# Performance work log

Hardware: AMD Instinct MI355X
Metric: run time of the kernel (lower is better)

## Reference

```python
import jax, jax.numpy as jnp
import numpy as np

EMBED_DIM = 1024
NUM_HEADS = 16
HEAD_DIM = EMBED_DIM // NUM_HEADS
BATCH, SEQ = 1, 4096


def setup_inputs() -> dict:
    key = jax.random.key(0)
    k1, k2, k3 = jax.random.split(key, 3)
    hidden_states = jax.random.normal(k1, (BATCH, SEQ, EMBED_DIM), dtype=jnp.float32)
    W_qkv = jax.random.normal(k2, (3 * EMBED_DIM, EMBED_DIM), dtype=jnp.float32) * 0.02
    b_qkv = jnp.zeros((3 * EMBED_DIM,), dtype=jnp.float32)
    # torch init: identity per head, perturb slightly to make test non-trivial
    eye = jnp.broadcast_to(jnp.eye(HEAD_DIM, dtype=jnp.float32), (NUM_HEADS, HEAD_DIM, HEAD_DIM))
    hebbian_trace = eye + 0.01 * jax.random.normal(k3, (NUM_HEADS, HEAD_DIM, HEAD_DIM), dtype=jnp.float32)
    return {"hidden_states": hidden_states, "W_qkv": W_qkv, "b_qkv": b_qkv, "hebbian_trace": hebbian_trace}


def reference(hidden_states, W_qkv, b_qkv, hebbian_trace):
    B, S, E = hidden_states.shape
    H, D = NUM_HEADS, HEAD_DIM
    qkv = hidden_states @ W_qkv.T + b_qkv              # [B,S,3E]
    q, k, v = jnp.split(qkv, 3, axis=-1)
    # [B,H,S,D]
    q = q.reshape(B, S, H, D).transpose(0, 2, 1, 3)
    k = k.reshape(B, S, H, D).transpose(0, 2, 1, 3)
    v = v.reshape(B, S, H, D).transpose(0, 2, 1, 3)
    scores = jnp.einsum('bhqd,bhkd->bhqk', q, k) / jnp.sqrt(jnp.float32(D))
    attn = jax.nn.softmax(scores, axis=-1)
    weighted_v = jnp.einsum('bhqk,bhkd->bhqd', attn, v)  # [B,H,S,D]
    # torch einsum 'blhd,hdd->blhd': repeated 'd' in trace -> diagonal scaling
    wv = weighted_v.transpose(0, 2, 1, 3)               # [B,S,H,D]
    v_transformed = jnp.einsum('blhd,hdd->blhd', wv, hebbian_trace)
    return v_transformed.reshape(B, S, E)
```

## Files before the change

kernel.cpp:

```cpp
#include <hip/hip_runtime.h>
#include <hip/hip_bf16.h>
#include <stdint.h>

#define S_LEN 4096

typedef short s16x8  __attribute__((ext_vector_type(8)));
typedef float f32x4  __attribute__((ext_vector_type(4)));
typedef float f32x16 __attribute__((ext_vector_type(16)));

#define CEXP 0.18033688011112042f

__device__ __forceinline__ unsigned short f2bf(float f) {
    union { float f; unsigned u; } v; v.f = f;
    unsigned r = v.u + 0x7fffu + ((v.u >> 16) & 1u);
    return (unsigned short)(r >> 16);
}

__device__ __forceinline__ ushort2 pkbf(float a, float b) {
    float2 f; f.x = a; f.y = b;
    __hip_bfloat162 h = __float22bfloat162_rn(f);
    union { __hip_bfloat162 h; ushort2 u; } cv; cv.h = h;
    return cv.u;
}

__device__ __forceinline__ ushort4 pkbf4(float x, float y, float z, float w) {
    ushort2 lo = pkbf(x, y), hi = pkbf(z, w);
    ushort4 r; r.x = lo.x; r.y = lo.y; r.z = hi.x; r.w = hi.y;
    return r;
}

__device__ __forceinline__ unsigned pku(float a, float b) {
    union { ushort2 s; unsigned u; } c; c.s = pkbf(a, b); return c.u;
}

typedef const __attribute__((address_space(1))) void* gas_t;
typedef __attribute__((address_space(3))) void* sas_t;

__device__ __forceinline__ void async16(const void* g, void* s) {
    __builtin_amdgcn_global_load_lds((gas_t)g, (sas_t)s, 16, 0, 0);
}

__global__ __launch_bounds__(256) void cvt_bf16(
    const float* __restrict__ X, const float* __restrict__ W,
    unsigned short* __restrict__ Xb, unsigned short* __restrict__ Wb)
{
    const long NX = 4194304;
    long i = (long)(blockIdx.x * 256 + threadIdx.x) * 8;
    const float* src; unsigned short* dst; long off;
    if (i < NX) { src = X; dst = Xb; off = i; }
    else        { src = W; dst = Wb; off = i - NX; }
    float4 a = *(const float4*)(src + off);
    float4 b = *(const float4*)(src + off + 4);
    union { s16x8 v; ushort4 q[2]; } o;
    o.q[0] = pkbf4(a.x, a.y, a.z, a.w);
    o.q[1] = pkbf4(b.x, b.y, b.z, b.w);
    *(s16x8*)(dst + off) = o.v;
}

__global__ __launch_bounds__(256) void qkv_gemm_bf16(
    const unsigned short* __restrict__ Xb, const unsigned short* __restrict__ Wb,
    const float* __restrict__ bias, const float* __restrict__ trace,
    unsigned short* __restrict__ Qb, unsigned short* __restrict__ Kb,
    unsigned short* __restrict__ Vt)
{
    __shared__ __align__(16) unsigned short sm[17408];
    unsigned short* As = sm;
    unsigned short* Bs = sm + 8192;

    const int t = threadIdx.x;
    const int l = t & 63;
    const int w = t >> 6;
    const int bm = blockIdx.y, bn = blockIdx.x;
    const int rowBase = (w >> 1) * 64;
    const int colBase = (w & 1) * 64;

    f32x4 acc[4][4];
#pragma unroll
    for (int i = 0; i < 4; i++)
#pragma unroll
        for (int j = 0; j < 4; j++) acc[i][j] = (f32x4)0.f;

    const int srow = l >> 3;
    const int scol = (l & 7) * 8;

    for (int kt = 0; kt < 16; ++kt) {
        const int k0 = kt * 64;
#pragma unroll
        for (int c = 0; c < 4; ++c) {
            int m = w * 4 + c;
            const unsigned short* ga = Xb + (bm * 128 + m * 8 + srow) * 1024 + k0 + scol;
            const unsigned short* gb = Wb + (bn * 128 + m * 8 + srow) * 1024 + k0 + scol;
            async16(ga, As + m * 512);
            async16(gb, Bs + m * 512);
        }
        __syncthreads();

#pragma unroll
        for (int kc = 0; kc < 2; ++kc) {
            s16x8 af[4], bf[4];
#pragma unroll
            for (int i = 0; i < 4; i++) {
                af[i] = *(const s16x8*)(As + (rowBase + i * 16 + (l & 15)) * 64 + kc * 32 + (l >> 4) * 8);
                bf[i] = *(const s16x8*)(Bs + (colBase + i * 16 + (l & 15)) * 64 + kc * 32 + (l >> 4) * 8);
            }
#pragma unroll
            for (int i = 0; i < 4; i++)
#pragma unroll
                for (int j = 0; j < 4; j++)
                    acc[i][j] = __builtin_amdgcn_mfma_f32_16x16x32_bf16(af[i], bf[j], acc[i][j], 0, 0, 0);
        }
        __syncthreads();
    }

    if (bn < 16) {
        unsigned short* Ls = sm;
        const int region = bn >> 3;
        unsigned short* dst = region ? Kb : Qb;
        const float scl = region ? 1.0f : CEXP;
#pragma unroll
        for (int j = 0; j < 4; j++) {
            int cl = colBase + j * 16 + (l & 15);
            float bv = bias[bn * 128 + cl];
#pragma unroll
            for (int i = 0; i < 4; i++) {
                int s0 = rowBase + i * 16 + ((l >> 4) << 2);
#pragma unroll
                for (int r = 0; r < 4; r++)
                    Ls[(s0 + r) * 136 + cl] = f2bf((acc[i][j][r] + bv) * scl);
            }
        }
        __syncthreads();
#pragma unroll
        for (int p = 0; p < 8; ++p) {
            int tk = p * 256 + t;
            int s  = tk >> 4;
            int ch = tk & 15;
            int gc = bn * 128 + ch * 8;
            int h  = (gc >> 6) & 15, d = gc & 63;
            s16x8 v = *(const s16x8*)(Ls + s * 136 + ch * 8);
            *(s16x8*)(dst + (h * S_LEN + bm * 128 + s) * 64 + d) = v;
        }
    } else {
        __syncthreads();
        unsigned short* Lt = sm;
#pragma unroll
        for (int j = 0; j < 4; j++) {
            int cl = colBase + j * 16 + (l & 15);
            int o  = bn * 128 + cl - 2048;
            float bv = bias[bn * 128 + cl];
            float tr = trace[(o >> 6) * 4096 + (o & 63) * 65];
#pragma unroll
            for (int i = 0; i < 4; i++) {
                int s0 = rowBase + i * 16 + ((l >> 4) << 2);
                *(ushort4*)(Lt + cl * 136 + s0) =
                    pkbf4((acc[i][j][0] + bv) * tr, (acc[i][j][1] + bv) * tr,
                          (acc[i][j][2] + bv) * tr, (acc[i][j][3] + bv) * tr);
            }
        }
        __syncthreads();
#pragma unroll
        for (int p = 0; p < 8; ++p) {
            int dl  = (t >> 4) + p * 16;
            int sch = (t & 15) * 8;
            int o = bn * 128 + dl - 2048;
            int h = o >> 6, d = o & 63;
            s16x8 v = *(const s16x8*)(Lt + dl * 136 + sch);
            *(s16x8*)(Vt + (h * 64 + d) * S_LEN + bm * 128 + sch) = v;
        }
    }
}

__global__ __launch_bounds__(256) void qkv_gemm_f32(
    const float* __restrict__ X, const float* __restrict__ W,
    const float* __restrict__ bias, const float* __restrict__ trace,
    unsigned short* __restrict__ Qb, unsigned short* __restrict__ Kb,
    unsigned short* __restrict__ Vt)
{
    __shared__ __align__(16) unsigned short sm[17408];
    unsigned short* As = sm;
    unsigned short* Bs = sm + 5120;

    const int t = threadIdx.x;
    const int l = t & 63;
    const int w = t >> 6;
    const int bm = blockIdx.y, bn = blockIdx.x;
    const int rowBase = (w >> 1) * 64;
    const int colBase = (w & 1) * 64;

    f32x4 acc[4][4];
#pragma unroll
    for (int i = 0; i < 4; i++)
#pragma unroll
        for (int j = 0; j < 4; j++) acc[i][j] = (f32x4)0.f;

    const int sr = t >> 3;
    const int sc = (t & 7) * 4;

    for (int kt = 0; kt < 32; ++kt) {
        const int k0 = kt * 32;
#pragma unroll
        for (int p = 0; p < 4; ++p) {
            int r = sr + p * 32;
            float4 xa = *(const float4*)(X + (bm * 128 + r) * 1024 + k0 + sc);
            float4 wb = *(const float4*)(W + (bn * 128 + r) * 1024 + k0 + sc);
            *(ushort4*)(As + r * 40 + sc) = pkbf4(xa.x, xa.y, xa.z, xa.w);
            *(ushort4*)(Bs + r * 40 + sc) = pkbf4(wb.x, wb.y, wb.z, wb.w);
        }
        __syncthreads();

        s16x8 af[4], bf[4];
#pragma unroll
        for (int i = 0; i < 4; i++) {
            af[i] = *(const s16x8*)(As + (rowBase + i * 16 + (l & 15)) * 40 + (l >> 4) * 8);
            bf[i] = *(const s16x8*)(Bs + (colBase + i * 16 + (l & 15)) * 40 + (l >> 4) * 8);
        }
#pragma unroll
        for (int i = 0; i < 4; i++)
#pragma unroll
            for (int j = 0; j < 4; j++)
                acc[i][j] = __builtin_amdgcn_mfma_f32_16x16x32_bf16(af[i], bf[j], acc[i][j], 0, 0, 0);
        __syncthreads();
    }

    if (bn < 16) {
#pragma unroll
        for (int j = 0; j < 4; j++) {
            int col = bn * 128 + colBase + j * 16 + (l & 15);
            float bv = bias[col];
            int region = col >> 10;
            int within = col & 1023;
            int h = within >> 6, d = within & 63;
            unsigned short* dst = (region == 0) ? Qb : Kb;
            float scl = (region == 0) ? CEXP : 1.0f;
#pragma unroll
            for (int i = 0; i < 4; i++) {
                int s0 = bm * 128 + rowBase + i * 16 + ((l >> 4) << 2);
#pragma unroll
                for (int r = 0; r < 4; r++)
                    dst[(h * S_LEN + s0 + r) * 64 + d] = f2bf((acc[i][j][r] + bv) * scl);
            }
        }
    } else {
        __syncthreads();
        unsigned short* Lt = sm;
#pragma unroll
        for (int j = 0; j < 4; j++) {
            int cl = colBase + j * 16 + (l & 15);
            int o  = bn * 128 + cl - 2048;
            float bv = bias[bn * 128 + cl];
            float tr = trace[(o >> 6) * 4096 + (o & 63) * 65];
#pragma unroll
            for (int i = 0; i < 4; i++) {
                int s0 = rowBase + i * 16 + ((l >> 4) << 2);
                *(ushort4*)(Lt + cl * 136 + s0) =
                    pkbf4((acc[i][j][0] + bv) * tr, (acc[i][j][1] + bv) * tr,
                          (acc[i][j][2] + bv) * tr, (acc[i][j][3] + bv) * tr);
            }
        }
        __syncthreads();
#pragma unroll
        for (int p = 0; p < 8; ++p) {
            int dl  = (t >> 4) + p * 16;
            int sch = (t & 15) * 8;
            int o = bn * 128 + dl - 2048;
            int h = o >> 6, d = o & 63;
            s16x8 v = *(const s16x8*)(Lt + dl * 136 + sch);
            *(s16x8*)(Vt + (h * 64 + d) * S_LEN + bm * 128 + sch) = v;
        }
    }
}

__global__ __launch_bounds__(512, 4) void attn(
    const unsigned short* __restrict__ Qb, const unsigned short* __restrict__ Kb,
    const unsigned short* __restrict__ Vt, float* __restrict__ out)
{
    __shared__ __align__(16) unsigned short sm[34816];
    __shared__ float lArr[256];

    const int t = threadIdx.x;
    const int l = t & 63;
    const int w = t >> 6;
    const int g = w >> 2;
    const int wg = w & 3;
    const int wq = w & 3;
    const int bid = blockIdx.x;
    const int xcd = bid & 7;
    const int j   = bid >> 3;
    const int h   = xcd * 2 + (j & 1);
    const int qblk = j >> 1;
    const int qbase = qblk * 128 + wq * 32;
    const int l31 = l & 31;
    const int lh  = l >> 5;
    const int swz = l31 & 7;

    s16x8 qf[4];
#pragma unroll
    for (int ks = 0; ks < 4; ks++)
        qf[ks] = *(const s16x8*)(Qb + (h * S_LEN + qbase + l31) * 64 + ks * 16 + lh * 8);

    f32x16 O0 = (f32x16)0.f, O1 = (f32x16)0.f;
    float2 lpA; lpA.x = 0.f; lpA.y = 0.f;
    float2 lpB; lpB.x = 0.f; lpB.y = 0.f;

    const int p0 = (wg * 2 + 0) * 64 + l;
    const int p1 = (wg * 2 + 1) * 64 + l;
    const int r0_ = p0 >> 3, c0_ = (p0 & 7) ^ (r0_ & 7);
    const int r1_ = p1 >> 3, c1_ = (p1 & 7) ^ (r1_ & 7);
    const unsigned short* gk0 = Kb + (h * S_LEN + g * 2048 + r0_) * 64 + c0_ * 8;
    const unsigned short* gk1 = Kb + (h * S_LEN + g * 2048 + r1_) * 64 + c1_ * 8;
    const unsigned short* gv0 = Vt + (h * 64 + r0_) * S_LEN + g * 2048 + c0_ * 8;
    const unsigned short* gv1 = Vt + (h * 64 + r1_) * S_LEN + g * 2048 + c1_ * 8;

    {
        unsigned short* kb_ = sm + g * 8192 + wg * 1024;
        async16(gk0, kb_);
        async16(gk1, kb_ + 512);
        async16(gv0, kb_ + 4096);
        async16(gv1, kb_ + 4096 + 512);
    }

    for (int kt = 0; kt < 32; ++kt) {
        __syncthreads();
        const unsigned short* sb  = sm + ((kt & 1) * 2 + g) * 8192;
        const unsigned short* vbs = sb + 4096;

        if (kt < 31) {
            gk0 += 4096; gk1 += 4096; gv0 += 64; gv1 += 64;
            unsigned short* kb_ = sm + (((kt + 1) & 1) * 2 + g) * 8192 + wg * 1024;
            async16(gk0, kb_);
            async16(gk1, kb_ + 512);
            async16(gv0, kb_ + 4096);
            async16(gv1, kb_ + 4096 + 512);
        }

        f32x16 S0 = (f32x16)0.f, S1 = (f32x16)0.f;
        __builtin_amdgcn_s_setprio(1);
#pragma unroll
        for (int ks = 0; ks < 4; ks++) {
            const int off = ((ks * 2 + lh) ^ swz) * 8;
            s16x8 a0 = *(const s16x8*)(sb + l31 * 64 + off);
            s16x8 a1 = *(const s16x8*)(sb + (32 + l31) * 64 + off);
            S0 = __builtin_amdgcn_mfma_f32_32x32x16_bf16(a0, qf[ks], S0, 0, 0, 0);
            S1 = __builtin_amdgcn_mfma_f32_32x32x16_bf16(a1, qf[ks], S1, 0, 0, 0);
        }
        __builtin_amdgcn_s_setprio(0);

#pragma unroll
        for (int i = 0; i < 16; i += 4) {
            float p0v = __builtin_amdgcn_exp2f(S0[i+0]); S0[i+0] = p0v; lpA.x += p0v;
            float p1v = __builtin_amdgcn_exp2f(S0[i+1]); S0[i+1] = p1v; lpA.y += p1v;
            float p2v = __builtin_amdgcn_exp2f(S0[i+2]); S0[i+2] = p2v; lpB.x += p2v;
            float p3v = __builtin_amdgcn_exp2f(S0[i+3]); S0[i+3] = p3v; lpB.y += p3v;
        }
#pragma unroll
        for (int i = 0; i < 16; i += 4) {
            float p0v = __builtin_amdgcn_exp2f(S1[i+0]); S1[i+0] = p0v; lpA.x += p0v;
            float p1v = __builtin_amdgcn_exp2f(S1[i+1]); S1[i+1] = p1v; lpA.y += p1v;
            float p2v = __builtin_amdgcn_exp2f(S1[i+2]); S1[i+2] = p2v; lpB.x += p2v;
            float p3v = __builtin_amdgcn_exp2f(S1[i+3]); S1[i+3] = p3v; lpB.y += p3v;
        }

        __builtin_amdgcn_s_setprio(1);
#define PVBLK(SX, BO, KS) do {                                               \
        unsigned pa0 = pku(SX[(BO)+0], SX[(BO)+1]);                          \
        unsigned pc0 = pku(SX[(BO)+4], SX[(BO)+5]);                          \
        unsigned pa1 = pku(SX[(BO)+2], SX[(BO)+3]);                          \
        unsigned pc1 = pku(SX[(BO)+6], SX[(BO)+7]);                          \
        auto r0 = __builtin_amdgcn_permlane32_swap(pa0, pc0, false, false);  \
        auto r1 = __builtin_amdgcn_permlane32_swap(pa1, pc1, false, false);  \
        union { s16x8 v; unsigned u[4]; } pb_;                               \
        pb_.u[0] = r0[0]; pb_.u[1] = r1[0]; pb_.u[2] = r0[1]; pb_.u[3] = r1[1]; \
        const int offv = (((KS) * 2 + lh) ^ swz) * 8;                        \
        s16x8 av0 = *(const s16x8*)(vbs + l31 * 64 + offv);                  \
        s16x8 av1 = *(const s16x8*)(vbs + (32 + l31) * 64 + offv);           \
        O0 = __builtin_amdgcn_mfma_f32_32x32x16_bf16(av0, pb_.v, O0, 0, 0, 0); \
        O1 = __builtin_amdgcn_mfma_f32_32x32x16_bf16(av1, pb_.v, O1, 0, 0, 0); \
    } while (0)
        PVBLK(S0, 0, 0);
        PVBLK(S0, 8, 1);
        PVBLK(S1, 0, 2);
        PVBLK(S1, 8, 3);
#undef PVBLK
        __builtin_amdgcn_s_setprio(0);
    }

    float l_part = (lpA.x + lpA.y) + (lpB.x + lpB.y);
    float l_tot = l_part + __shfl_xor(l_part, 32);
    if (lh == 0) lArr[w * 32 + l31] = l_tot;

    __syncthreads();

    float* Lo = (float*)sm + w * 2176;
#pragma unroll
    for (int dt = 0; dt < 2; ++dt) {
        const f32x16& Ox = dt ? O1 : O0;
#pragma unroll
        for (int gq = 0; gq < 4; ++gq) {
            int d0 = dt * 32 + gq * 8 + lh * 4;
            float4 vv;
            vv.x = Ox[gq*4+0]; vv.y = Ox[gq*4+1]; vv.z = Ox[gq*4+2]; vv.w = Ox[gq*4+3];
            *(float4*)(Lo + l31 * 68 + d0) = vv;
        }
    }
    __syncthreads();

    if (w < 4) {
        const float* LoA = (float*)sm + w * 2176;
        const float* LoB = (float*)sm + (w + 4) * 2176;
#pragma unroll
        for (int it = 0; it < 8; ++it) {
            int ql = it * 4 + (l >> 4);
            float invl = 1.0f / (lArr[w * 32 + ql] + lArr[(w + 4) * 32 + ql]);
            float4 a = *(const float4*)(LoA + ql * 68 + (l & 15) * 4);
            float4 b = *(const float4*)(LoB + ql * 68 + (l & 15) * 4);
            float4 vv;
            vv.x = (a.x + b.x) * invl;
            vv.y = (a.y + b.y) * invl;
            vv.z = (a.z + b.z) * invl;
            vv.w = (a.w + b.w) * invl;
            *(float4*)(out + (qblk * 128 + w * 32 + ql) * 1024 + h * 64 + (l & 15) * 4) = vv;
        }
    }
}

extern "C" void kernel_launch(void* const* d_in, const int* in_sizes, int n_in,
                              void* d_out, int out_size, void* d_ws, size_t ws_size,
                              hipStream_t stream) {
    const float* X     = (const float*)d_in[0];
    const float* W     = (const float*)d_in[1];
    const float* bias  = (const float*)d_in[2];
    const float* trace = (const float*)d_in[3];
    float* out = (float*)d_out;

    unsigned short* Qb = (unsigned short*)d_ws;
    unsigned short* Kb = Qb + 4194304;
    unsigned short* Vt = Kb + 4194304;
    unsigned short* Xb = Vt + 4194304;
    unsigned short* Wb = Xb + 4194304;

    const size_t NEED_BF16 = (size_t)3 * 8388608 + 8388608 + 6291456;

    if (ws_size >= NEED_BF16) {
        cvt_bf16<<<3584, 256, 0, stream>>>(X, W, Xb, Wb);
        qkv_gemm_bf16<<<dim3(24, 32), 256, 0, stream>>>(Xb, Wb, bias, trace, Qb, Kb, Vt);
    } else {
        qkv_gemm_f32<<<dim3(24, 32), 256, 0, stream>>>(X, W, bias, trace, Qb, Kb, Vt);
    }
    attn<<<512, 512, 0, stream>>>(Qb, Kb, Vt, out);
}
```

Before: 206.8 us.

## Double-buffer QKV GEMM shared-memory tiles to overlap loads with MFMA

The QKV projection GEMM now uses two LDS buffers with a K-tile of 32 instead of 64. It prefetches the next tile asynchronously while MFMAs run on the current one, and needs only one barrier per iteration. The goal is to hide global-to-LDS load latency that the old load-sync-compute-sync loop left exposed. The cost is twice as many iterations and barriers, less MFMA work per barrier, and a different LDS row stride that may change bank-conflict behaviour.

After: 194.7 us (median of 2 runs). -5.9%, faster.

```diff
diff --git a/kernel.cpp b/kernel.cpp
--- a/kernel.cpp
+++ b/kernel.cpp
@@ -64,8 +64,6 @@
     unsigned short* __restrict__ Vt)
 {
     __shared__ __align__(16) unsigned short sm[17408];
-    unsigned short* As = sm;
-    unsigned short* Bs = sm + 8192;
 
     const int t = threadIdx.x;
     const int l = t & 63;
@@ -80,37 +78,44 @@
 #pragma unroll
         for (int j = 0; j < 4; j++) acc[i][j] = (f32x4)0.f;
 
-    const int srow = l >> 3;
-    const int scol = (l & 7) * 8;
-
-    for (int kt = 0; kt < 16; ++kt) {
-        const int k0 = kt * 64;
-#pragma unroll
-        for (int c = 0; c < 4; ++c) {
-            int m = w * 4 + c;
-            const unsigned short* ga = Xb + (bm * 128 + m * 8 + srow) * 1024 + k0 + scol;
-            const unsigned short* gb = Wb + (bn * 128 + m * 8 + srow) * 1024 + k0 + scol;
-            async16(ga, As + m * 512);
-            async16(gb, Bs + m * 512);
-        }
-        __syncthreads();
-
-#pragma unroll
-        for (int kc = 0; kc < 2; ++kc) {
-            s16x8 af[4], bf[4];
-#pragma unroll
-            for (int i = 0; i < 4; i++) {
-                af[i] = *(const s16x8*)(As + (rowBase + i * 16 + (l & 15)) * 64 + kc * 32 + (l >> 4) * 8);
-                bf[i] = *(const s16x8*)(Bs + (colBase + i * 16 + (l & 15)) * 64 + kc * 32 + (l >> 4) * 8);
-            }
-#pragma unroll
-            for (int i = 0; i < 4; i++)
-#pragma unroll
-                for (int j = 0; j < 4; j++)
-                    acc[i][j] = __builtin_amdgcn_mfma_f32_16x16x32_bf16(af[i], bf[j], acc[i][j], 0, 0, 0);
-        }
-        __syncthreads();
-    }
+    const int p0 = w * 128 + l;
+    const int p1 = p0 + 64;
+    const int ar0 = p0 >> 2, ac0 = (p0 & 3) * 8;
+    const int ar1 = p1 >> 2, ac1 = (p1 & 3) * 8;
+
+    async16(Xb + (bm * 128 + ar0) * 1024 + ac0, sm + p0 * 8);
+    async16(Xb + (bm * 128 + ar1) * 1024 + ac1, sm + p1 * 8);
+    async16(Wb + (bn * 128 + ar0) * 1024 + ac0, sm + 4096 + p0 * 8);
+    async16(Wb + (bn * 128 + ar1) * 1024 + ac1, sm + 4096 + p1 * 8);
+
+    for (int kt = 0; kt < 32; ++kt) {
+        __syncthreads();
+        const unsigned short* As = sm + (kt & 1) * 8192;
+        const unsigned short* Bs = As + 4096;
+
+        if (kt < 31) {
+            const int k0 = (kt + 1) * 32;
+            unsigned short* An = sm + ((kt + 1) & 1) * 8192;
+            async16(Xb + (bm * 128 + ar0) * 1024 + k0 + ac0, An + p0 * 8);
+            async16(Xb + (bm * 128 + ar1) * 1024 + k0 + ac1, An + p1 * 8);
+            async16(Wb + (bn * 128 + ar0) * 1024 + k0 + ac0, An + 4096 + p0 * 8);
+            async16(Wb + (bn * 128 + ar1) * 1024 + k0 + ac1, An + 4096 + p1 * 8);
+        }
+
+        s16x8 af[4], bf[4];
+#pragma unroll
+        for (int i = 0; i < 4; i++) {
+            af[i] = *(const s16x8*)(As + (rowBase + i * 16 + (l & 15)) * 32 + (l >> 4) * 8);
+            bf[i] = *(const s16x8*)(Bs + (colBase + i * 16 + (l & 15)) * 32 + (l >> 4) * 8);
+        }
+#pragma unroll
+        for (int i = 0; i < 4; i++)
+#pragma unroll
+            for (int j = 0; j < 4; j++)
+                acc[i][j] = __builtin_amdgcn_mfma_f32_16x16x32_bf16(af[i], bf[j], acc[i][j], 0, 0, 0);
+    }
+
+    __syncthreads();
 
     if (bn < 16) {
         unsigned short* Ls = sm;
@@ -141,7 +146,6 @@
             *(s16x8*)(dst + (h * S_LEN + bm * 128 + s) * 64 + d) = v;
         }
     } else {
-        __syncthreads();
         unsigned short* Lt = sm;
 #pragma unroll
         for (int j = 0; j < 4; j++) {
```
